# Performance work log

Measured on AMD Instinct MI355X. Metric: run time of the kernel, lower is better.

The kernel has to match this reference:

```python
import jax, jax.numpy as jnp
import numpy as np

# Rows of A/B form separable 3x3 filters via outer product:
#   f0 = identity, f1 = sobel_y, f2 = sobel_x
_A = np.array([[0, 1, 0], [1, 0, -1], [1, 2, 1]], dtype=np.float32)
_B = np.array([[0, 1, 0], [1, 2, 1], [1, 0, -1]], dtype=np.float32)
_LAP = np.array([[0, -1, 0], [-1, 4, -1], [0, -1, 0]], dtype=np.float32)  # 4-connected Laplacian


def _fixed_kernels(C):
    # separable depthwise kernels, torch grouped-conv channel-major order: out idx = c*3 + f
    sep = np.einsum('fi,fj->fij', _A, _B)                       # (3, 3, 3)
    sep_k = np.tile(sep[None], (C, 1, 1, 1)).reshape(C * 3, 1, 3, 3)
    lap_k = np.tile(_LAP[None, None], (C, 1, 1, 1))             # (C, 1, 3, 3)
    return jnp.asarray(sep_k), jnp.asarray(lap_k)


def _conv(xp, k, groups=1):
    # cross-correlation, VALID on already-padded input (matches torch F.conv2d)
    return jax.lax.conv_general_dilated(
        xp, k, window_strides=(1, 1), padding='VALID',
        dimension_numbers=('NCHW', 'OIHW', 'NCHW'),
        feature_group_count=groups)


def setup_inputs() -> dict:
    key = jax.random.key(0)
    k1, k2, k3 = jax.random.split(key, 3)
    N, C, H, W, F = 8, 64, 256, 256, 128
    x = jax.random.normal(k1, (N, C, H, W), dtype=jnp.float32)
    fan_in = C * 9
    W_learned = jax.random.uniform(k2, (F, C, 3, 3), jnp.float32,
                                   -1.0 / np.sqrt(fan_in), 1.0 / np.sqrt(fan_in))
    b_learned = jax.random.uniform(k3, (F,), jnp.float32,
                                   -1.0 / np.sqrt(fan_in), 1.0 / np.sqrt(fan_in))
    return {"x": x, "W_learned": W_learned, "b_learned": b_learned}


def reference(x, W_learned, b_learned):
    C = x.shape[1]
    sep_k, lap_k = _fixed_kernels(C)
    # replicate (edge) pad by 1 on H and W
    xp = jnp.pad(x, ((0, 0), (0, 0), (1, 1), (1, 1)), mode='edge')
    sep = _conv(xp, sep_k, groups=C)                 # (N, 3C, H, W)
    lap = _conv(xp, lap_k, groups=C)                 # (N, C,  H, W)
    learned = _conv(xp, W_learned) + b_learned[None, :, None, None]  # (N, F, H, W)
    return jnp.concatenate([sep, lap, learned], axis=1)
```

## Files before the change

### kernel.cpp

```cpp
#include <hip/hip_runtime.h>

#define HH 256
#define WW 256
#define CC 64
#define FF 128
#define NN 8
#define OUTC 384
#define HW (HH * WW)

typedef __attribute__((ext_vector_type(8))) short bf16x8;
typedef __attribute__((ext_vector_type(4))) float f32x4;

__device__ __forceinline__ int clampi(int v, int lo, int hi) {
    return v < lo ? lo : (v > hi ? hi : v);
}

static __device__ __forceinline__ unsigned short f2bf(float x) {
    unsigned u = __builtin_bit_cast(unsigned, x);
    u += 0x7FFFu + ((u >> 16) & 1u);
    return (unsigned short)(u >> 16);
}
static __device__ __forceinline__ unsigned packbf(float a, float b) {
    return (unsigned)f2bf(a) | ((unsigned)f2bf(b) << 16);
}
static __device__ __forceinline__ float bf2f(unsigned short s) {
    return __builtin_bit_cast(float, (unsigned)s << 16);
}
static __device__ __forceinline__ void nts(float* p, float a, float b, float c, float d) {
    f32x4 v = {a, b, c, d};
    __builtin_nontemporal_store(v, reinterpret_cast<f32x4*>(p));
}

__global__ __launch_bounds__(256) void wT_kernel(const float* __restrict__ Wl,
                                                 unsigned short* __restrict__ wsW) {
    int e = blockIdx.x * 256 + threadIdx.x;
    if (e >= 9216) return;
    int t = e >> 10;
    int rem = e & 1023;
    int kg = rem >> 7;
    int f = rem & 127;
    unsigned u[4];
#pragma unroll
    for (int j2 = 0; j2 < 4; ++j2) {
        float a = Wl[(size_t)f * 576 + (size_t)(kg * 8 + 2 * j2) * 9 + t];
        float b = Wl[(size_t)f * 576 + (size_t)(kg * 8 + 2 * j2 + 1) * 9 + t];
        u[j2] = packbf(a, b);
    }
    *reinterpret_cast<uint4*>(wsW + (size_t)e * 8) = make_uint4(u[0], u[1], u[2], u[3]);
}

__global__ __launch_bounds__(256) void pack_kernel(const float* __restrict__ x,
                                                   unsigned short* __restrict__ xt) {
    int b = blockIdx.x;
    int y = b & 255;
    int cg = (b >> 8) & 7;
    int n = b >> 11;
    int w = threadIdx.x;
    const float* xp = x + ((size_t)(n * CC + cg * 8)) * HW + (size_t)y * WW + w;
    unsigned u[4];
#pragma unroll
    for (int j2 = 0; j2 < 4; ++j2)
        u[j2] = packbf(xp[(size_t)(2 * j2) * HW], xp[(size_t)(2 * j2 + 1) * HW]);
    *reinterpret_cast<uint4*>(xt + ((size_t)((n * 8 + cg) * HH + y) * WW + w) * 8) =
        make_uint4(u[0], u[1], u[2], u[3]);
}

__global__ __launch_bounds__(256, 4) void fused_kernel(const unsigned short* __restrict__ wsW,
                                                       const unsigned short* __restrict__ xt,
                                                       const float* __restrict__ bl,
                                                       float* __restrict__ out) {
    __shared__ float lds_e[4][16][68];

    int bid = blockIdx.x;
    int q = ((bid & 7) << 9) | (bid >> 3);
    int xs = q & 1;
    int y = (q >> 1) & 255;
    int n = q >> 9;

    int tid = threadIdx.x;
    int lane = tid & 63;
    int w = tid >> 6;
    int wf = w >> 1;
    int ws = w & 1;
    int x0 = xs * 128 + ws * 64;
    int lr = lane & 15;
    int lk = lane >> 4;

    const char* xb = reinterpret_cast<const char*>(xt) + (size_t)n * (8 * HH * WW * 16);

    int colb[4][3];
#pragma unroll
    for (int j = 0; j < 4; ++j)
#pragma unroll
        for (int dx = 0; dx < 3; ++dx)
            colb[j][dx] = clampi(x0 + j * 16 + lr + dx - 1, 0, WW - 1) * 16;

    int pxg = x0 + lane;
    int dwyr[3], dwwc[3];
#pragma unroll
    for (int d = 0; d < 3; ++d) {
        dwyr[d] = clampi(y + d - 1, 0, HH - 1);
        dwwc[d] = clampi(pxg + d - 1, 0, WW - 1);
    }

    f32x4 acc[4][4] = {};

#pragma unroll
    for (int t = 0; t < 9; ++t) {
        int dy = t / 3, dx = t - 3 * (t / 3);
        int yc = clampi(y + dy - 1, 0, HH - 1);
#pragma unroll
        for (int kk = 0; kk < 2; ++kk) {
            int kg = kk * 4 + lk;
            size_t rowoff = ((size_t)kg * HH + yc) * (WW * 16);
            bf16x8 a4[4], b4[4];
#pragma unroll
            for (int mt = 0; mt < 4; ++mt)
                a4[mt] = *reinterpret_cast<const bf16x8*>(
                    wsW + ((size_t)(t * 8 + kg) * 128 + wf * 64 + mt * 16 + lr) * 8);
#pragma unroll
            for (int j = 0; j < 4; ++j)
                b4[j] = *reinterpret_cast<const bf16x8*>(xb + rowoff + colb[j][dx]);
#pragma unroll
            for (int mt = 0; mt < 4; ++mt)
#pragma unroll
                for (int j = 0; j < 4; ++j)
                    acc[mt][j] = __builtin_amdgcn_mfma_f32_16x16x32_bf16(
                        a4[mt], b4[j], acc[mt][j], 0, 0, 0);
        }

        if (t < 8) {
            int cg = t;
            const char* cgbase = xb + (size_t)cg * HH * (WW * 16) + wf * 8;
            uint2 c9[3][3];
#pragma unroll
            for (int r = 0; r < 3; ++r)
#pragma unroll
                for (int d = 0; d < 3; ++d)
                    c9[r][d] = *reinterpret_cast<const uint2*>(
                        cgbase + ((size_t)dwyr[r] * WW + dwwc[d]) * 16);
            size_t ob = (size_t)n * OUTC * HW + (size_t)y * WW + pxg;
#pragma unroll
            for (int i = 0; i < 4; ++i) {
                float v[3][3];
#pragma unroll
                for (int r = 0; r < 3; ++r)
#pragma unroll
                    for (int d = 0; d < 3; ++d) {
                        unsigned word = (i < 2) ? c9[r][d].x : c9[r][d].y;
                        v[r][d] = bf2f((unsigned short)((i & 1) ? (word >> 16) : (word & 0xffff)));
                    }
                int ch = cg * 8 + wf * 4 + i;
                float o0 = v[1][1];
                float o1 = (v[0][0] + 2.f * v[0][1] + v[0][2]) - (v[2][0] + 2.f * v[2][1] + v[2][2]);
                float o2 = (v[0][0] - v[0][2]) + 2.f * (v[1][0] - v[1][2]) + (v[2][0] - v[2][2]);
                float o3 = 4.f * v[1][1] - v[0][1] - v[2][1] - v[1][0] - v[1][2];
                __builtin_nontemporal_store(o0, out + ob + (size_t)(ch * 3 + 0) * HW);
                __builtin_nontemporal_store(o1, out + ob + (size_t)(ch * 3 + 1) * HW);
                __builtin_nontemporal_store(o2, out + ob + (size_t)(ch * 3 + 2) * HW);
                __builtin_nontemporal_store(o3, out + ob + (size_t)(192 + ch) * HW);
            }
        }
    }

    float* le = &lds_e[w][0][0];
#pragma unroll
    for (int mt = 0; mt < 4; ++mt) {
#pragma unroll
        for (int i = 0; i < 4; ++i) {
            int f16 = lk * 4 + i;
            float bv = bl[wf * 64 + mt * 16 + f16];
#pragma unroll
            for (int j = 0; j < 4; ++j)
                le[f16 * 68 + j * 16 + lr] = acc[mt][j][i] + bv;
        }
#pragma unroll
        for (int p = 0; p < 4; ++p) {
            int f16 = p * 4 + lk;
            const float* s = &le[f16 * 68 + lr * 4];
            int f = wf * 64 + mt * 16 + f16;
            nts(out + (size_t)(n * OUTC + 256 + f) * HW + (size_t)y * WW + x0 + lr * 4,
                s[0], s[1], s[2], s[3]);
        }
    }
}

extern "C" void kernel_launch(void* const* d_in, const int* in_sizes, int n_in,
                              void* d_out, int out_size, void* d_ws, size_t ws_size,
                              hipStream_t stream) {
    const float* x  = (const float*)d_in[0];
    const float* Wl = (const float*)d_in[1];
    const float* bl = (const float*)d_in[2];
    float* out = (float*)d_out;

    unsigned short* wsW = (unsigned short*)d_ws;
    unsigned short* xt  = (unsigned short*)((char*)d_ws + 262144);

    wT_kernel<<<36, 256, 0, stream>>>(Wl, wsW);
    pack_kernel<<<16384, 256, 0, stream>>>(x, xt);
    fused_kernel<<<NN * 512, 256, 0, stream>>>(wsW, xt, bl, out);
}
```

Measured before the change: 255.9 us.

## Widen blocks to full rows and compute depthwise outputs from fp32 input

```diff
diff --git a/kernel.cpp b/kernel.cpp
--- a/kernel.cpp
+++ b/kernel.cpp
@@ -23,10 +23,7 @@
 static __device__ __forceinline__ unsigned packbf(float a, float b) {
     return (unsigned)f2bf(a) | ((unsigned)f2bf(b) << 16);
 }
-static __device__ __forceinline__ float bf2f(unsigned short s) {
-    return __builtin_bit_cast(float, (unsigned)s << 16);
-}
-static __device__ __forceinline__ void nts(float* p, float a, float b, float c, float d) {
+static __device__ __forceinline__ void nts4(float* p, float a, float b, float c, float d) {
     f32x4 v = {a, b, c, d};
     __builtin_nontemporal_store(v, reinterpret_cast<f32x4*>(p));
 }
@@ -65,43 +62,39 @@
         make_uint4(u[0], u[1], u[2], u[3]);
 }
 
-__global__ __launch_bounds__(256, 4) void fused_kernel(const unsigned short* __restrict__ wsW,
+__global__ __launch_bounds__(512, 4) void fused_kernel(const unsigned short* __restrict__ wsW,
                                                        const unsigned short* __restrict__ xt,
+                                                       const float* __restrict__ x,
                                                        const float* __restrict__ bl,
                                                        float* __restrict__ out) {
-    __shared__ float lds_e[4][16][68];
+    __shared__ float lds_e[32][260];
 
     int bid = blockIdx.x;
-    int q = ((bid & 7) << 9) | (bid >> 3);
-    int xs = q & 1;
-    int y = (q >> 1) & 255;
-    int n = q >> 9;
+    int q = ((bid & 7) << 8) | (bid >> 3);
+    int y = q & 255;
+    int n = q >> 8;
 
     int tid = threadIdx.x;
     int lane = tid & 63;
     int w = tid >> 6;
-    int wf = w >> 1;
-    int ws = w & 1;
-    int x0 = xs * 128 + ws * 64;
+    int wf = w >> 2;
+    int wq = w & 3;
+    int x0 = wq * 64;
     int lr = lane & 15;
     int lk = lane >> 4;
 
     const char* xb = reinterpret_cast<const char*>(xt) + (size_t)n * (8 * HH * WW * 16);
 
-    int colb[4][3];
-#pragma unroll
-    for (int j = 0; j < 4; ++j)
-#pragma unroll
-        for (int dx = 0; dx < 3; ++dx)
-            colb[j][dx] = clampi(x0 + j * 16 + lr + dx - 1, 0, WW - 1) * 16;
-
-    int pxg = x0 + lane;
-    int dwyr[3], dwwc[3];
-#pragma unroll
-    for (int d = 0; d < 3; ++d) {
-        dwyr[d] = clampi(y + d - 1, 0, HH - 1);
-        dwwc[d] = clampi(pxg + d - 1, 0, WW - 1);
-    }
+    int colx[4];
+#pragma unroll
+    for (int j = 0; j < 4; ++j) colx[j] = x0 + j * 16 + lr;
+
+    int px0 = lane * 4;
+    int pa = px0 >= 4 ? px0 - 4 : 0;
+    int pc = px0 <= 248 ? px0 + 4 : 252;
+    int yr[3];
+#pragma unroll
+    for (int d = 0; d < 3; ++d) yr[d] = clampi(y + d - 1, 0, HH - 1);
 
     f32x4 acc[4][4] = {};
 
@@ -109,6 +102,9 @@
     for (int t = 0; t < 9; ++t) {
         int dy = t / 3, dx = t - 3 * (t / 3);
         int yc = clampi(y + dy - 1, 0, HH - 1);
+        int cb[4];
+#pragma unroll
+        for (int j = 0; j < 4; ++j) cb[j] = clampi(colx[j] + dx - 1, 0, WW - 1) * 16;
 #pragma unroll
         for (int kk = 0; kk < 2; ++kk) {
             int kg = kk * 4 + lk;
@@ -120,7 +116,7 @@
                     wsW + ((size_t)(t * 8 + kg) * 128 + wf * 64 + mt * 16 + lr) * 8);
 #pragma unroll
             for (int j = 0; j < 4; ++j)
-                b4[j] = *reinterpret_cast<const bf16x8*>(xb + rowoff + colb[j][dx]);
+                b4[j] = *reinterpret_cast<const bf16x8*>(xb + rowoff + cb[j]);
 #pragma unroll
             for (int mt = 0; mt < 4; ++mt)
 #pragma unroll
@@ -130,58 +126,65 @@
         }
 
         if (t < 8) {
-            int cg = t;
-            const char* cgbase = xb + (size_t)cg * HH * (WW * 16) + wf * 8;
-            uint2 c9[3][3];
-#pragma unroll
-            for (int r = 0; r < 3; ++r)
-#pragma unroll
-                for (int d = 0; d < 3; ++d)
-                    c9[r][d] = *reinterpret_cast<const uint2*>(
-                        cgbase + ((size_t)dwyr[r] * WW + dwwc[d]) * 16);
-            size_t ob = (size_t)n * OUTC * HW + (size_t)y * WW + pxg;
-#pragma unroll
-            for (int i = 0; i < 4; ++i) {
-                float v[3][3];
-#pragma unroll
-                for (int r = 0; r < 3; ++r)
-#pragma unroll
-                    for (int d = 0; d < 3; ++d) {
-                        unsigned word = (i < 2) ? c9[r][d].x : c9[r][d].y;
-                        v[r][d] = bf2f((unsigned short)((i & 1) ? (word >> 16) : (word & 0xffff)));
-                    }
-                int ch = cg * 8 + wf * 4 + i;
-                float o0 = v[1][1];
-                float o1 = (v[0][0] + 2.f * v[0][1] + v[0][2]) - (v[2][0] + 2.f * v[2][1] + v[2][2]);
-                float o2 = (v[0][0] - v[0][2]) + 2.f * (v[1][0] - v[1][2]) + (v[2][0] - v[2][2]);
-                float o3 = 4.f * v[1][1] - v[0][1] - v[2][1] - v[1][0] - v[1][2];
-                __builtin_nontemporal_store(o0, out + ob + (size_t)(ch * 3 + 0) * HW);
-                __builtin_nontemporal_store(o1, out + ob + (size_t)(ch * 3 + 1) * HW);
-                __builtin_nontemporal_store(o2, out + ob + (size_t)(ch * 3 + 2) * HW);
-                __builtin_nontemporal_store(o3, out + ob + (size_t)(192 + ch) * HW);
+            int c = t * 8 + w;
+            const float* xc = x + ((size_t)(n * CC + c)) * HW;
+            float lv[3], rv[3];
+            float4 Bv[3];
+#pragma unroll
+            for (int r = 0; r < 3; ++r) {
+                const float* rp = xc + (size_t)yr[r] * WW;
+                float4 A = *(const float4*)(rp + pa);
+                float4 B = *(const float4*)(rp + px0);
+                float4 C = *(const float4*)(rp + pc);
+                lv[r] = px0 ? A.w : B.x;
+                rv[r] = (px0 < 252) ? C.x : B.w;
+                Bv[r] = B;
             }
+            float o0[4], o1[4], o2[4], o3[4];
+#pragma unroll
+            for (int j = 0; j < 4; ++j) {
+                float tL = j ? (&Bv[0].x)[j - 1] : lv[0];
+                float tC = (&Bv[0].x)[j];
+                float tR = (j < 3) ? (&Bv[0].x)[j + 1] : rv[0];
+                float mL = j ? (&Bv[1].x)[j - 1] : lv[1];
+                float mC = (&Bv[1].x)[j];
+                float mR = (j < 3) ? (&Bv[1].x)[j + 1] : rv[1];
+                float bL = j ? (&Bv[2].x)[j - 1] : lv[2];
+                float bC = (&Bv[2].x)[j];
+                float bR = (j < 3) ? (&Bv[2].x)[j + 1] : rv[2];
+                o0[j] = mC;
+                o1[j] = (tL + 2.f * tC + tR) - (bL + 2.f * bC + bR);
+                o2[j] = (tL - tR) + 2.f * (mL - mR) + (bL - bR);
+                o3[j] = 4.f * mC - tC - bC - mL - mR;
+            }
+            float* ob = out + (size_t)n * OUTC * HW + (size_t)y * WW + px0;
+            nts4(ob + (size_t)(c * 3 + 0) * HW, o0[0], o0[1], o0[2], o0[3]);
+            nts4(ob + (size_t)(c * 3 + 1) * HW, o1[0], o1[1], o1[2], o1[3]);
+            nts4(ob + (size_t)(c * 3 + 2) * HW, o2[0], o2[1], o2[2], o2[3]);
+            nts4(ob + (size_t)(192 + c)   * HW, o3[0], o3[1], o3[2], o3[3]);
         }
     }
 
-    float* le = &lds_e[w][0][0];
 #pragma unroll
     for (int mt = 0; mt < 4; ++mt) {
 #pragma unroll
         for (int i = 0; i < 4; ++i) {
-            int f16 = lk * 4 + i;
-            float bv = bl[wf * 64 + mt * 16 + f16];
+            int fp = wf * 16 + lk * 4 + i;
+            float bv = bl[wf * 64 + mt * 16 + lk * 4 + i];
 #pragma unroll
             for (int j = 0; j < 4; ++j)
-                le[f16 * 68 + j * 16 + lr] = acc[mt][j][i] + bv;
-        }
+                lds_e[fp][x0 + j * 16 + lr] = acc[mt][j][i] + bv;
+        }
+        __syncthreads();
 #pragma unroll
         for (int p = 0; p < 4; ++p) {
-            int f16 = p * 4 + lk;
-            const float* s = &le[f16 * 68 + lr * 4];
-            int f = wf * 64 + mt * 16 + f16;
-            nts(out + (size_t)(n * OUTC + 256 + f) * HW + (size_t)y * WW + x0 + lr * 4,
-                s[0], s[1], s[2], s[3]);
-        }
+            int fp = w * 4 + p;
+            int f = (fp >> 4) * 64 + mt * 16 + (fp & 15);
+            const float* s = &lds_e[fp][lane * 4];
+            nts4(out + (size_t)(n * OUTC + 256 + f) * HW + (size_t)y * WW + lane * 4,
+                 s[0], s[1], s[2], s[3]);
+        }
+        __syncthreads();
     }
 }
 
@@ -198,5 +201,5 @@
 
     wT_kernel<<<36, 256, 0, stream>>>(Wl, wsW);
     pack_kernel<<<16384, 256, 0, stream>>>(x, xt);
-    fused_kernel<<<NN * 512, 256, 0, stream>>>(wsW, xt, bl, out);
-}
+    fused_kernel<<<2048, 512, 0, stream>>>(wsW, xt, x, bl, out);
+}
```

Measured after the change: 353.2 us. +38.0%, slower.
